# Performance work log

Hardware: AMD Instinct MI355X
Metric: run time of the kernel (lower is better)

## Reference

```python
import jax, jax.numpy as jnp
import numpy as np

N, D, DH, H = 2048, 256, 256, 4
DHEAD = DH // H
NEG = -1e30


def setup_inputs() -> dict:
    key = jax.random.key(0)
    ks = jax.random.split(key, 24)
    s = 0.05
    inp = {
        'axiom_states': jax.random.normal(ks[0], (N, D), jnp.float32),
        'adj0': (jax.random.uniform(ks[1], (N, N)) < 0.015).astype(jnp.float32),
        'adj1': (jax.random.uniform(ks[2], (N, N)) < 0.015).astype(jnp.float32),
        'w0': jax.random.uniform(ks[3], (N, N), jnp.float32),
        'w1': jax.random.uniform(ks[4], (N, N), jnp.float32),
        'Wm0': jax.random.normal(ks[5], (DH, D), jnp.float32) * s,
        'bm0': jax.random.normal(ks[6], (DH,), jnp.float32) * s,
        'Wa0': jax.random.normal(ks[7], (H, 2 * D), jnp.float32) * s,
        'ba0': jax.random.normal(ks[8], (H,), jnp.float32) * s,
        'Wm1': jax.random.normal(ks[9], (DH, D), jnp.float32) * s,
        'bm1': jax.random.normal(ks[10], (DH,), jnp.float32) * s,
        'Wa1': jax.random.normal(ks[11], (H, 2 * D), jnp.float32) * s,
        'ba1': jax.random.normal(ks[12], (H,), jnp.float32) * s,
        'gru_wih': jax.random.normal(ks[13], (3 * D, 2 * DH), jnp.float32) * s,
        'gru_whh': jax.random.normal(ks[14], (3 * D, D), jnp.float32) * s,
        'gru_bih': jax.random.normal(ks[15], (3 * D,), jnp.float32) * s,
        'gru_bhh': jax.random.normal(ks[16], (3 * D,), jnp.float32) * s,
        'ln_g': jnp.ones((D,), jnp.float32),
        'ln_b': jnp.zeros((D,), jnp.float32),
    }
    return inp


def _edge_messages(x, adj, w, Wm, bm, Wa, ba):
    # GAT-style decomposition of Linear([x_i, x_j]) -> a_cur[i] + a_nb[j] + b
    a_cur = x @ Wa[:, :D].T                      # [N,H] (target i, first half of concat)
    a_nb = x @ Wa[:, D:].T                       # [N,H] (neighbor j, second half)
    s = a_nb[:, None, :] + a_cur[None, :, :] + ba  # [j,i,H]
    s = jax.nn.leaky_relu(s, 0.2)
    s = s * w[:, :, None]                        # edge-weight scaled scores (pre-softmax)
    mask = adj != 0                              # edge j -> i iff adj[j,i] != 0
    logits = jnp.where(mask[:, :, None], s, NEG)
    attn = jax.nn.softmax(logits, axis=0) * mask[:, :, None]  # zero for isolated nodes
    msg = (x @ Wm.T + bm).reshape(N, H, DHEAD)   # per-neighbor messages
    agg = jnp.einsum('jih,jhd->ihd', attn, msg)  # softmax-weighted sum over neighbors
    return agg.reshape(N, DH)


def _forward(axiom_states, adj0, adj1, w0, w1, Wm0, bm0, Wa0, ba0,
             Wm1, bm1, Wa1, ba1, gru_wih, gru_whh, gru_bih, gru_bhh, ln_g, ln_b):
    m0 = _edge_messages(axiom_states, adj0, w0, Wm0, bm0, Wa0, ba0)
    m1 = _edge_messages(axiom_states, adj1, w1, Wm1, bm1, Wa1, ba1)
    msg = jnp.concatenate([m0, m1], axis=-1)     # dropout is identity in eval
    # GRUCell (torch semantics)
    gi = msg @ gru_wih.T + gru_bih
    gh = axiom_states @ gru_whh.T + gru_bhh
    r = jax.nn.sigmoid(gi[:, :D] + gh[:, :D])
    z = jax.nn.sigmoid(gi[:, D:2 * D] + gh[:, D:2 * D])
    n = jnp.tanh(gi[:, 2 * D:] + r * gh[:, 2 * D:])
    h = (1.0 - z) * n + z * axiom_states
    # LayerNorm
    mu = jnp.mean(h, axis=-1, keepdims=True)
    var = jnp.var(h, axis=-1, keepdims=True)
    return (h - mu) * jax.lax.rsqrt(var + 1e-5) * ln_g + ln_b


def reference(axiom_states, adj0, adj1, w0, w1, Wm0, bm0, Wa0, ba0,
              Wm1, bm1, Wa1, ba1, gru_wih, gru_whh, gru_bih, gru_bhh, ln_g, ln_b):
    return _forward(axiom_states, adj0, adj1, w0, w1, Wm0, bm0, Wa0, ba0,
                    Wm1, bm1, Wa1, ba1, gru_wih, gru_whh, gru_bih, gru_bhh, ln_g, ln_b)
```

## Files before the change

### kernel.cpp

```cpp
#include <hip/hip_runtime.h>

#define NN 2048
#define DD 256
#define HH 4
#define ECAP 128

typedef unsigned short ushort_t;
typedef __attribute__((ext_vector_type(4))) unsigned short us4;
typedef __attribute__((ext_vector_type(8))) unsigned short us8;
typedef __attribute__((ext_vector_type(8))) short s8;
typedef __attribute__((ext_vector_type(4))) float f4;

__device__ __forceinline__ ushort_t f2b(float f) {
    unsigned int u = __float_as_uint(f);
    return (ushort_t)((u + 0x7fffu + ((u >> 16) & 1u)) >> 16);
}
__device__ __forceinline__ float b2f(ushort_t b) {
    return __uint_as_float(((unsigned int)b) << 16);
}
__device__ __forceinline__ void gl_lds16(const void* g, void* l) {
    __builtin_amdgcn_global_load_lds(
        (const __attribute__((address_space(1))) void*)g,
        (__attribute__((address_space(3))) void*)l, 16, 0, 0);
}

__device__ __forceinline__ void gemm_core_db(
    const ushort_t* __restrict__ A, int lda, const ushort_t* __restrict__ B, int ldb,
    int r0, int c0, int K, ushort_t (*as)[64], ushort_t (*bs)[64], f4 acc[2][2])
{
    const int t = threadIdx.x;
    const int wave = t >> 6, lane = t & 63;
    const int wm = (wave & 1) * 32, wn = (wave >> 1) * 32;
    const int fm = lane & 15, fq = lane >> 4;

    const int m0q0 = wave * 16 + (lane >> 3);
    const int m0q1 = m0q0 + 8;
    const int cs0 = ((lane & 7) ^ (m0q0 & 7)) * 8;
    const int cs1 = ((lane & 7) ^ (m0q1 & 7)) * 8;
    const ushort_t* ga0 = A + (size_t)(r0 + m0q0) * lda + cs0;
    const ushort_t* ga1 = A + (size_t)(r0 + m0q1) * lda + cs1;
    const ushort_t* gb0 = B + (size_t)(c0 + m0q0) * ldb + cs0;
    const ushort_t* gb1 = B + (size_t)(c0 + m0q1) * ldb + cs1;
    const int ra0 = wm + fm, ra1 = wm + 16 + fm;
    const int rb0 = wn + fm, rb1 = wn + 16 + fm;

    gl_lds16(ga0, &as[wave * 16][0]);
    gl_lds16(ga1, &as[wave * 16 + 8][0]);
    gl_lds16(gb0, &bs[wave * 16][0]);
    gl_lds16(gb1, &bs[wave * 16 + 8][0]);
    __syncthreads();

    int buf = 0;
    for (int k0 = 0; k0 < K; k0 += 64) {
        const int nb = buf ^ 64;
        if (k0 + 64 < K) {
            gl_lds16(ga0 + k0 + 64, &as[nb + wave * 16][0]);
            gl_lds16(ga1 + k0 + 64, &as[nb + wave * 16 + 8][0]);
            gl_lds16(gb0 + k0 + 64, &bs[nb + wave * 16][0]);
            gl_lds16(gb1 + k0 + 64, &bs[nb + wave * 16 + 8][0]);
        }
        #pragma unroll
        for (int kk = 0; kk < 2; ++kk) {
            const int cc = kk * 4 + fq;
            const s8 a0 = *(const s8*)&as[buf + ra0][(cc ^ (ra0 & 7)) * 8];
            const s8 a1 = *(const s8*)&as[buf + ra1][(cc ^ (ra1 & 7)) * 8];
            const s8 b0 = *(const s8*)&bs[buf + rb0][(cc ^ (rb0 & 7)) * 8];
            const s8 b1 = *(const s8*)&bs[buf + rb1][(cc ^ (rb1 & 7)) * 8];
            acc[0][0] = __builtin_amdgcn_mfma_f32_16x16x32_bf16(a0, b0, acc[0][0], 0, 0, 0);
            acc[0][1] = __builtin_amdgcn_mfma_f32_16x16x32_bf16(a0, b1, acc[0][1], 0, 0, 0);
            acc[1][0] = __builtin_amdgcn_mfma_f32_16x16x32_bf16(a1, b0, acc[1][0], 0, 0, 0);
            acc[1][1] = __builtin_amdgcn_mfma_f32_16x16x32_bf16(a1, b1, acc[1][1], 0, 0, 0);
        }
        __syncthreads();
        buf = nb;
    }
}

__device__ __forceinline__ us8 cvt8(float4 a, float4 b) {
    us8 o;
    o[0] = f2b(a.x); o[1] = f2b(a.y); o[2] = f2b(a.z); o[3] = f2b(a.w);
    o[4] = f2b(b.x); o[5] = f2b(b.y); o[6] = f2b(b.z); o[7] = f2b(b.w);
    return o;
}

__device__ __forceinline__ void gemm_core_f32(
    const float* __restrict__ A, int lda, const float* __restrict__ B, int ldb,
    int r0, int c0, int K, ushort_t (*as)[64], ushort_t (*bs)[64], f4 acc[2][2])
{
    const int t = threadIdx.x;
    const int wave = t >> 6, lane = t & 63;
    const int wm = (wave & 1) * 32, wn = (wave >> 1) * 32;
    const int fm = lane & 15, fq = lane >> 4;

    const int m1 = wave * 16 + (lane >> 3);
    const int m2 = m1 + 8;
    const int g1 = ((lane & 7) ^ (m1 & 7)) * 8;
    const int g2 = ((lane & 7) ^ (m2 & 7)) * 8;
    const int cl = (lane & 7) * 8;
    const int ra0 = wm + fm, ra1 = wm + 16 + fm;
    const int rb0 = wn + fm, rb1 = wn + 16 + fm;

    const float* pa1 = A + (size_t)(r0 + m1) * lda + g1;
    const float* pa2 = A + (size_t)(r0 + m2) * lda + g2;
    const float* pb1 = B + (size_t)(c0 + m1) * ldb + g1;
    const float* pb2 = B + (size_t)(c0 + m2) * ldb + g2;

    float4 aa0 = *(const float4*)(pa1);
    float4 aa1 = *(const float4*)(pa1 + 4);
    float4 ab0 = *(const float4*)(pa2);
    float4 ab1 = *(const float4*)(pa2 + 4);
    float4 ba0 = *(const float4*)(pb1);
    float4 ba1 = *(const float4*)(pb1 + 4);
    float4 bb0 = *(const float4*)(pb2);
    float4 bb1 = *(const float4*)(pb2 + 4);

    for (int k0 = 0; k0 < K; k0 += 64) {
        __syncthreads();
        *(us8*)&as[m1][cl] = cvt8(aa0, aa1);
        *(us8*)&as[m2][cl] = cvt8(ab0, ab1);
        *(us8*)&bs[m1][cl] = cvt8(ba0, ba1);
        *(us8*)&bs[m2][cl] = cvt8(bb0, bb1);
        __syncthreads();
        if (k0 + 64 < K) {
            aa0 = *(const float4*)(pa1 + k0 + 64);
            aa1 = *(const float4*)(pa1 + k0 + 68);
            ab0 = *(const float4*)(pa2 + k0 + 64);
            ab1 = *(const float4*)(pa2 + k0 + 68);
            ba0 = *(const float4*)(pb1 + k0 + 64);
            ba1 = *(const float4*)(pb1 + k0 + 68);
            bb0 = *(const float4*)(pb2 + k0 + 64);
            bb1 = *(const float4*)(pb2 + k0 + 68);
        }
        #pragma unroll
        for (int kk = 0; kk < 2; ++kk) {
            const int cc = kk * 4 + fq;
            const s8 a0 = *(const s8*)&as[ra0][(cc ^ (ra0 & 7)) * 8];
            const s8 a1 = *(const s8*)&as[ra1][(cc ^ (ra1 & 7)) * 8];
            const s8 b0 = *(const s8*)&bs[rb0][(cc ^ (rb0 & 7)) * 8];
            const s8 b1 = *(const s8*)&bs[rb1][(cc ^ (rb1 & 7)) * 8];
            acc[0][0] = __builtin_amdgcn_mfma_f32_16x16x32_bf16(a0, b0, acc[0][0], 0, 0, 0);
            acc[0][1] = __builtin_amdgcn_mfma_f32_16x16x32_bf16(a0, b1, acc[0][1], 0, 0, 0);
            acc[1][0] = __builtin_amdgcn_mfma_f32_16x16x32_bf16(a1, b0, acc[1][0], 0, 0, 0);
            acc[1][1] = __builtin_amdgcn_mfma_f32_16x16x32_bf16(a1, b1, acc[1][1], 0, 0, 0);
        }
    }
}

#define E_SC  256
#define E_AP  384
#define E_WI  768
#define E_NB  1408

__global__ __launch_bounds__(256) void fused1_kernel(
    const float* __restrict__ x,
    const float* __restrict__ adj0, const float* __restrict__ adj1,
    const float* __restrict__ Wm0, const float* __restrict__ Wm1,
    const float* __restrict__ whh, const float* __restrict__ wih,
    const float* __restrict__ Wa0, const float* __restrict__ Wa1,
    const float* __restrict__ bm0, const float* __restrict__ bm1,
    const float* __restrict__ bhh,
    int* __restrict__ cnt, int* __restrict__ ej,
    ushort_t* __restrict__ wihb,
    float* __restrict__ acur, float* __restrict__ anb,
    ushort_t* __restrict__ msgb, float* __restrict__ gh)
{
    __shared__ char smem[16448];
    const int b = blockIdx.x, t = threadIdx.x;

    if (b < E_SC) {
        const int l = b & 1, chunk = b >> 1;
        const int i0 = chunk * 16;
        const float* adj = l ? adj1 : adj0;
        int* lcnt = (int*)smem;
        if (t < 16) lcnt[t] = 0;
        __syncthreads();
        const int rowLane = t >> 2, q = t & 3;
        for (int r0r = 0; r0r < NN; r0r += 512) {
            float4 a[8];
            #pragma unroll
            for (int it = 0; it < 8; ++it) {
                const int j = r0r + it * 64 + rowLane;
                a[it] = *(const float4*)(adj + (size_t)j * NN + i0 + q * 4);
            }
            #pragma unroll
            for (int it = 0; it < 8; ++it) {
                const int j = r0r + it * 64 + rowLane;
                const float av[4] = {a[it].x, a[it].y, a[it].z, a[it].w};
                #pragma unroll
                for (int u = 0; u < 4; ++u) {
                    if (av[u] != 0.f) {
                        const int li = q * 4 + u;
                        const int slot = atomicAdd(&lcnt[li], 1);
                        if (slot < ECAP)
                            ej[((size_t)l * NN + i0 + li) * ECAP + slot] = j;
                    }
                }
            }
        }
        __syncthreads();
        if (t < 16) cnt[l * NN + i0 + t] = min(lcnt[t], ECAP);
        return;
    }
    if (b < E_AP) {
        float* sh = (float*)smem;
        const int i0 = (b - E_SC) * 16;
        for (int rr = 0; rr < 16; ++rr)
            sh[rr * 257 + t] = x[(size_t)(i0 + rr) * DD + t];
        __syncthreads();
        const int r = t >> 4, idx = t & 15;
        const int l = idx >> 3, isnb = (idx >> 2) & 1, h = idx & 3;
        const float* wrow = (l ? Wa1 : Wa0) + h * (2 * DD) + isnb * DD;
        float acc = 0.f;
        for (int k = 0; k < DD; ++k) acc = fmaf(sh[r * 257 + k], wrow[k], acc);
        float* dst = isnb ? anb : acur;
        dst[((size_t)l * NN + i0 + r) * HH + h] = acc;
        return;
    }
    if (b < E_WI) {
        const int id = (b - E_AP) * 1024 + t * 4;
        const float4 v = *(const float4*)(wih + id);
        us4 o; o.x = f2b(v.x); o.y = f2b(v.y); o.z = f2b(v.z); o.w = f2b(v.w);
        *(us4*)(wihb + id) = o;
        return;
    }
    {
        ushort_t (*as)[64] = (ushort_t(*)[64])smem;
        ushort_t (*bs)[64] = (ushort_t(*)[64])(smem + 8192);
        const int wave = t >> 6, lane = t & 63;
        const int wm = (wave & 1) * 32, wn = (wave >> 1) * 32;
        const int fm = lane & 15, fq = lane >> 4;
        const int idx = b - E_WI;
        const int c0 = (idx % 20) * 64, r0 = (idx / 20) * 64;
        const float* Bsrc = (c0 < 256) ? Wm0 + (size_t)c0 * DD
                          : (c0 < 512) ? Wm1 + (size_t)(c0 - 256) * DD
                                       : whh + (size_t)(c0 - 512) * DD;
        f4 acc[2][2] = {};
        gemm_core_f32(x, DD, Bsrc, DD, r0, 0, DD, as, bs, acc);
        #pragma unroll
        for (int ni = 0; ni < 2; ++ni) {
            const int col = c0 + wn + ni * 16 + fm;
            const float bv = (col < 256) ? bm0[col]
                           : (col < 512) ? bm1[col - 256]
                                         : bhh[col - 512];
            #pragma unroll
            for (int mi = 0; mi < 2; ++mi) {
                #pragma unroll
                for (int r = 0; r < 4; ++r) {
                    const int row = r0 + wm + mi * 16 + fq * 4 + r;
                    const float v = acc[mi][ni][r] + bv;
                    if (col < 512) msgb[(size_t)row * 512 + col] = f2b(v);
                    else           gh[(size_t)row * 768 + col - 512] = v;
                }
            }
        }
    }
}

__global__ __launch_bounds__(256) void attn_kernel(
    const int* __restrict__ cnt, const int* __restrict__ ej,
    const float* __restrict__ w0, const float* __restrict__ w1,
    const float* __restrict__ acur, const float* __restrict__ anb,
    const float* __restrict__ ba0, const float* __restrict__ ba1,
    const ushort_t* __restrict__ msgb, ushort_t* __restrict__ mcatb)
{
    const int i = blockIdx.x, l = blockIdx.y, t = threadIdx.x;
    __shared__ float es[HH][ECAP];
    __shared__ int ejs[ECAP];
    const int ne = min(max(cnt[l * NN + i], 0), ECAP);
    const float* ba = l ? ba1 : ba0;
    const float* w  = l ? w1 : w0;
    const size_t ebase = ((size_t)l * NN + i) * ECAP;

    if (t < ne) {
        const int j = ej[ebase + t];
        const float wv = w[(size_t)j * NN + i];
        ejs[t] = j;
        const float4 av = *(const float4*)(anb + ((size_t)l * NN + j) * HH);
        const float sv[4] = {av.x, av.y, av.z, av.w};
        #pragma unroll
        for (int h = 0; h < HH; ++h) {
            float s = sv[h] + acur[((size_t)l * NN + i) * HH + h] + ba[h];
            s = (s > 0.f) ? s : 0.2f * s;
            es[h][t] = s * wv;
        }
    }
    __syncthreads();
    {
        const int h = t >> 6, lane = t & 63;
        float s0 = (lane < ne) ? es[h][lane] : -1e30f;
        float s1 = (lane + 64 < ne) ? es[h][lane + 64] : -1e30f;
        float m = fmaxf(s0, s1);
        #pragma unroll
        for (int off = 32; off; off >>= 1) m = fmaxf(m, __shfl_xor(m, off));
        const float p0 = expf(s0 - m), p1 = expf(s1 - m);
        float sum = p0 + p1;
        #pragma unroll
        for (int off = 32; off; off >>= 1) sum += __shfl_xor(sum, off);
        const float inv = (ne > 0) ? 1.f / sum : 0.f;
        es[h][lane] = p0 * inv;
        if (lane + 64 < ECAP) es[h][lane + 64] = p1 * inv;
    }
    __syncthreads();
    const int h = t >> 6;
    const int off = l * DD + t;
    float acc = 0.f;
    int e = 0;
    for (; e + 8 <= ne; e += 8) {
        float v[8];
        #pragma unroll
        for (int u = 0; u < 8; ++u)
            v[u] = b2f(msgb[(size_t)ejs[e + u] * 512 + off]);
        #pragma unroll
        for (int u = 0; u < 8; ++u)
            acc = fmaf(es[h][e + u], v[u], acc);
    }
    for (; e < ne; ++e)
        acc = fmaf(es[h][e], b2f(msgb[(size_t)ejs[e] * 512 + off]), acc);
    mcatb[(size_t)i * (2 * DD) + off] = f2b(acc);
}

__global__ __launch_bounds__(256) void gemm2_kernel(
    const ushort_t* __restrict__ mcatb, const ushort_t* __restrict__ wihb,
    const float* __restrict__ bih, float* __restrict__ gi)
{
    __shared__ ushort_t as[128][64];
    __shared__ ushort_t bs[128][64];
    const int t = threadIdx.x;
    const int wave = t >> 6, lane = t & 63;
    const int wm = (wave & 1) * 32, wn = (wave >> 1) * 32;
    const int fm = lane & 15, fq = lane >> 4;
    const int c0 = blockIdx.x * 64, r0 = blockIdx.y * 64;
    f4 acc[2][2] = {};
    gemm_core_db(mcatb, 512, wihb, 512, r0, c0, 512, as, bs, acc);
    #pragma unroll
    for (int ni = 0; ni < 2; ++ni) {
        const int col = c0 + wn + ni * 16 + fm;
        const float bv = bih[col];
        #pragma unroll
        for (int mi = 0; mi < 2; ++mi)
            #pragma unroll
            for (int r = 0; r < 4; ++r)
                gi[(size_t)(r0 + wm + mi * 16 + fq * 4 + r) * 768 + col] =
                    acc[mi][ni][r] + bv;
    }
}

__global__ __launch_bounds__(256) void gates_ln(
    const float* __restrict__ gi, const float* __restrict__ gh, const float* __restrict__ x,
    const float* __restrict__ lng, const float* __restrict__ lnb, float* __restrict__ out)
{
    const int t = threadIdx.x;
    const int lane = t & 63, wv = t >> 6;
    const int row = blockIdx.x * 4 + wv;
    const size_t b768 = (size_t)row * 768;
    const int c = lane * 4;
    const f4 gir = *(const f4*)(gi + b768 + c);
    const f4 giz = *(const f4*)(gi + b768 + 256 + c);
    const f4 gin = *(const f4*)(gi + b768 + 512 + c);
    const f4 ghr = *(const f4*)(gh + b768 + c);
    const f4 ghz = *(const f4*)(gh + b768 + 256 + c);
    const f4 ghn = *(const f4*)(gh + b768 + 512 + c);
    const f4 xv  = *(const f4*)(x + (size_t)row * DD + c);
    f4 hv;
    float s1 = 0.f, s2 = 0.f;
    #pragma unroll
    for (int u = 0; u < 4; ++u) {
        const float rr = 1.f / (1.f + expf(-(gir[u] + ghr[u])));
        const float zz = 1.f / (1.f + expf(-(giz[u] + ghz[u])));
        const float nn = tanhf(gin[u] + rr * ghn[u]);
        const float h = (1.f - zz) * nn + zz * xv[u];
        hv[u] = h;
        s1 += h;
        s2 += h * h;
    }
    #pragma unroll
    for (int off = 32; off; off >>= 1) {
        s1 += __shfl_xor(s1, off);
        s2 += __shfl_xor(s2, off);
    }
    const float mu  = s1 * (1.f / DD);
    const float var = s2 * (1.f / DD) - mu * mu;
    const float inv = rsqrtf(var + 1e-5f);
    const f4 gv = *(const f4*)(lng + c);
    const f4 bv = *(const f4*)(lnb + c);
    f4 res;
    #pragma unroll
    for (int u = 0; u < 4; ++u)
        res[u] = (hv[u] - mu) * inv * gv[u] + bv[u];
    *(f4*)(out + (size_t)row * DD + c) = res;
}

extern "C" void kernel_launch(void* const* d_in, const int* in_sizes, int n_in,
                              void* d_out, int out_size, void* d_ws, size_t ws_size,
                              hipStream_t stream)
{
    const float* x    = (const float*)d_in[0];
    const float* adj0 = (const float*)d_in[1];
    const float* adj1 = (const float*)d_in[2];
    const float* w0   = (const float*)d_in[3];
    const float* w1   = (const float*)d_in[4];
    const float* Wm0  = (const float*)d_in[5];
    const float* bm0  = (const float*)d_in[6];
    const float* Wa0  = (const float*)d_in[7];
    const float* ba0  = (const float*)d_in[8];
    const float* Wm1  = (const float*)d_in[9];
    const float* bm1  = (const float*)d_in[10];
    const float* Wa1  = (const float*)d_in[11];
    const float* ba1  = (const float*)d_in[12];
    const float* wih  = (const float*)d_in[13];
    const float* whh  = (const float*)d_in[14];
    const float* bih  = (const float*)d_in[15];
    const float* bhh  = (const float*)d_in[16];
    const float* lng  = (const float*)d_in[17];
    const float* lnb  = (const float*)d_in[18];
    float* out = (float*)d_out;

    float* ws = (float*)d_ws;
    float* gh   = ws;            ws += (size_t)NN * 768;
    float* gi   = ws;            ws += (size_t)NN * 768;
    float* acur = ws;            ws += 2 * NN * HH;
    float* anb  = ws;            ws += 2 * NN * HH;
    int*   cnt  = (int*)ws;      ws += 2 * NN;
    int*   ej   = (int*)ws;      ws += 2 * NN * ECAP;
    ushort_t* wihb  = (ushort_t*)ws;  ws += (size_t)768 * 512 / 2;
    ushort_t* msgb  = (ushort_t*)ws;  ws += (size_t)NN * 512 / 2;
    ushort_t* mcatb = (ushort_t*)ws;  ws += (size_t)NN * 512 / 2;

    fused1_kernel<<<E_NB, 256, 0, stream>>>(
        x, adj0, adj1, Wm0, Wm1, whh, wih, Wa0, Wa1, bm0, bm1, bhh,
        cnt, ej, wihb, acur, anb, msgb, gh);
    attn_kernel<<<dim3(NN, 2), 256, 0, stream>>>(
        cnt, ej, w0, w1, acur, anb, ba0, ba1, msgb, mcatb);
    gemm2_kernel<<<dim3(12, 32), 256, 0, stream>>>(mcatb, wihb, bih, gi);
    gates_ln<<<NN / 4, 256, 0, stream>>>(gi, gh, x, lng, lnb, out);
}
```

Baseline: 167.6 us.

## Merge four kernels into one persistent kernel with grid-wide barriers

```diff
diff --git a/kernel.cpp b/kernel.cpp
--- a/kernel.cpp
+++ b/kernel.cpp
@@ -4,6 +4,7 @@
 #define DD 256
 #define HH 4
 #define ECAP 128
+#define NBLK 512
 
 typedef unsigned short ushort_t;
 typedef __attribute__((ext_vector_type(4))) unsigned short us4;
@@ -22,6 +23,18 @@
     __builtin_amdgcn_global_load_lds(
         (const __attribute__((address_space(1))) void*)g,
         (__attribute__((address_space(3))) void*)l, 16, 0, 0);
+}
+
+__device__ __forceinline__ void gsync(int* bar) {
+    __threadfence();
+    __syncthreads();
+    if (threadIdx.x == 0) {
+        __hip_atomic_fetch_add(bar, 1, __ATOMIC_ACQ_REL, __HIP_MEMORY_SCOPE_AGENT);
+        while (__hip_atomic_load(bar, __ATOMIC_ACQUIRE, __HIP_MEMORY_SCOPE_AGENT) < NBLK)
+            __builtin_amdgcn_s_sleep(1);
+    }
+    __syncthreads();
+    __threadfence();
 }
 
 __device__ __forceinline__ void gemm_core_db(
@@ -151,243 +164,273 @@
 #define E_WI  768
 #define E_NB  1408
 
-__global__ __launch_bounds__(256) void fused1_kernel(
+__global__ __launch_bounds__(256, 2) void mega_kernel(
     const float* __restrict__ x,
     const float* __restrict__ adj0, const float* __restrict__ adj1,
+    const float* __restrict__ w0, const float* __restrict__ w1,
     const float* __restrict__ Wm0, const float* __restrict__ Wm1,
     const float* __restrict__ whh, const float* __restrict__ wih,
     const float* __restrict__ Wa0, const float* __restrict__ Wa1,
     const float* __restrict__ bm0, const float* __restrict__ bm1,
     const float* __restrict__ bhh,
+    const float* __restrict__ ba0, const float* __restrict__ ba1,
+    const float* __restrict__ bih,
+    const float* __restrict__ lng, const float* __restrict__ lnb,
     int* __restrict__ cnt, int* __restrict__ ej,
     ushort_t* __restrict__ wihb,
     float* __restrict__ acur, float* __restrict__ anb,
-    ushort_t* __restrict__ msgb, float* __restrict__ gh)
+    ushort_t* __restrict__ msgb, ushort_t* __restrict__ mcatb,
+    float* __restrict__ gh, float* __restrict__ gi,
+    float* __restrict__ out, int* __restrict__ bar)
 {
-    __shared__ char smem[16448];
-    const int b = blockIdx.x, t = threadIdx.x;
-
-    if (b < E_SC) {
-        const int l = b & 1, chunk = b >> 1;
-        const int i0 = chunk * 16;
-        const float* adj = l ? adj1 : adj0;
-        int* lcnt = (int*)smem;
-        if (t < 16) lcnt[t] = 0;
+    __shared__ __align__(16) char smem[32768];
+    const int rb = blockIdx.x, t = threadIdx.x;
+
+    for (int vb = rb; vb < E_NB; vb += NBLK) {
+        if (vb < E_SC) {
+            const int l = vb & 1, chunk = vb >> 1;
+            const int i0 = chunk * 16;
+            const float* adj = l ? adj1 : adj0;
+            int* lcnt = (int*)smem;
+            if (t < 16) lcnt[t] = 0;
+            __syncthreads();
+            const int rowLane = t >> 2, q = t & 3;
+            for (int r0r = 0; r0r < NN; r0r += 512) {
+                float4 a[8];
+                #pragma unroll
+                for (int it = 0; it < 8; ++it) {
+                    const int j = r0r + it * 64 + rowLane;
+                    a[it] = *(const float4*)(adj + (size_t)j * NN + i0 + q * 4);
+                }
+                #pragma unroll
+                for (int it = 0; it < 8; ++it) {
+                    const int j = r0r + it * 64 + rowLane;
+                    const float av[4] = {a[it].x, a[it].y, a[it].z, a[it].w};
+                    #pragma unroll
+                    for (int u = 0; u < 4; ++u) {
+                        if (av[u] != 0.f) {
+                            const int li = q * 4 + u;
+                            const int slot = atomicAdd(&lcnt[li], 1);
+                            if (slot < ECAP)
+                                ej[((size_t)l * NN + i0 + li) * ECAP + slot] = j;
+                        }
+                    }
+                }
+            }
+            __syncthreads();
+            if (t < 16) cnt[l * NN + i0 + t] = min(lcnt[t], ECAP);
+        } else if (vb < E_AP) {
+            float* sh = (float*)smem;
+            const int i0 = (vb - E_SC) * 16;
+            for (int rr = 0; rr < 16; ++rr)
+                sh[rr * 257 + t] = x[(size_t)(i0 + rr) * DD + t];
+            __syncthreads();
+            const int r = t >> 4, idx = t & 15;
+            const int l = idx >> 3, isnb = (idx >> 2) & 1, h = idx & 3;
+            const float* wrow = (l ? Wa1 : Wa0) + h * (2 * DD) + isnb * DD;
+            float acc = 0.f;
+            for (int k = 0; k < DD; ++k) acc = fmaf(sh[r * 257 + k], wrow[k], acc);
+            float* dst = isnb ? anb : acur;
+            dst[((size_t)l * NN + i0 + r) * HH + h] = acc;
+        } else if (vb < E_WI) {
+            const int id = (vb - E_AP) * 1024 + t * 4;
+            const float4 v = *(const float4*)(wih + id);
+            us4 o; o.x = f2b(v.x); o.y = f2b(v.y); o.z = f2b(v.z); o.w = f2b(v.w);
+            *(us4*)(wihb + id) = o;
+        } else {
+            ushort_t (*as)[64] = (ushort_t(*)[64])smem;
+            ushort_t (*bs)[64] = (ushort_t(*)[64])(smem + 8192);
+            const int wave = t >> 6, lane = t & 63;
+            const int wm = (wave & 1) * 32, wn = (wave >> 1) * 32;
+            const int fm = lane & 15, fq = lane >> 4;
+            const int idx = vb - E_WI;
+            const int c0 = (idx % 20) * 64, r0 = (idx / 20) * 64;
+            const float* Bsrc = (c0 < 256) ? Wm0 + (size_t)c0 * DD
+                              : (c0 < 512) ? Wm1 + (size_t)(c0 - 256) * DD
+                                           : whh + (size_t)(c0 - 512) * DD;
+            f4 acc[2][2] = {};
+            gemm_core_f32(x, DD, Bsrc, DD, r0, 0, DD, as, bs, acc);
+            #pragma unroll
+            for (int ni = 0; ni < 2; ++ni) {
+                const int col = c0 + wn + ni * 16 + fm;
+                const float bv = (col < 256) ? bm0[col]
+                               : (col < 512) ? bm1[col - 256]
+                                             : bhh[col - 512];
+                #pragma unroll
+                for (int mi = 0; mi < 2; ++mi) {
+                    #pragma unroll
+                    for (int r = 0; r < 4; ++r) {
+                        const int row = r0 + wm + mi * 16 + fq * 4 + r;
+                        const float v = acc[mi][ni][r] + bv;
+                        if (col < 512) msgb[(size_t)row * 512 + col] = f2b(v);
+                        else           gh[(size_t)row * 768 + col - 512] = v;
+                    }
+                }
+            }
+        }
         __syncthreads();
-        const int rowLane = t >> 2, q = t & 3;
-        for (int r0r = 0; r0r < NN; r0r += 512) {
-            float4 a[8];
+    }
+    gsync(bar + 0);
+
+    {
+        const int wave = t >> 6, lane = t & 63;
+        float (*esw)[ECAP] = (float(*)[ECAP])smem + wave * HH;
+        int* ejs = (int*)(smem + 8192) + wave * ECAP;
+        for (int it = 0; it < 2; ++it) {
+            const int pair = it * 2048 + rb * 4 + wave;
+            const int i = pair & (NN - 1), l = pair >> 11;
+            const int ne = min(max(cnt[l * NN + i], 0), ECAP);
+            const float* ba = l ? ba1 : ba0;
+            const float* w  = l ? w1 : w0;
+            const size_t ebase = ((size_t)l * NN + i) * ECAP;
+            float acv[4];
             #pragma unroll
-            for (int it = 0; it < 8; ++it) {
-                const int j = r0r + it * 64 + rowLane;
-                a[it] = *(const float4*)(adj + (size_t)j * NN + i0 + q * 4);
+            for (int h = 0; h < HH; ++h)
+                acv[h] = acur[((size_t)l * NN + i) * HH + h];
+
+            float s0[HH], s1[HH];
+            int j0 = 0, j1 = 0;
+            if (lane < ne) {
+                j0 = ej[ebase + lane];
+                const float wv = w[(size_t)j0 * NN + i];
+                const float4 av = *(const float4*)(anb + ((size_t)l * NN + j0) * HH);
+                const float sv[4] = {av.x, av.y, av.z, av.w};
+                #pragma unroll
+                for (int h = 0; h < HH; ++h) {
+                    float s = sv[h] + acv[h] + ba[h];
+                    s = (s > 0.f) ? s : 0.2f * s;
+                    s0[h] = s * wv;
+                }
+            } else {
+                #pragma unroll
+                for (int h = 0; h < HH; ++h) s0[h] = -1e30f;
+            }
+            if (lane + 64 < ne) {
+                j1 = ej[ebase + lane + 64];
+                const float wv = w[(size_t)j1 * NN + i];
+                const float4 av = *(const float4*)(anb + ((size_t)l * NN + j1) * HH);
+                const float sv[4] = {av.x, av.y, av.z, av.w};
+                #pragma unroll
+                for (int h = 0; h < HH; ++h) {
+                    float s = sv[h] + acv[h] + ba[h];
+                    s = (s > 0.f) ? s : 0.2f * s;
+                    s1[h] = s * wv;
+                }
+            } else {
+                #pragma unroll
+                for (int h = 0; h < HH; ++h) s1[h] = -1e30f;
             }
             #pragma unroll
-            for (int it = 0; it < 8; ++it) {
-                const int j = r0r + it * 64 + rowLane;
-                const float av[4] = {a[it].x, a[it].y, a[it].z, a[it].w};
-                #pragma unroll
-                for (int u = 0; u < 4; ++u) {
-                    if (av[u] != 0.f) {
-                        const int li = q * 4 + u;
-                        const int slot = atomicAdd(&lcnt[li], 1);
-                        if (slot < ECAP)
-                            ej[((size_t)l * NN + i0 + li) * ECAP + slot] = j;
-                    }
-                }
-            }
-        }
-        __syncthreads();
-        if (t < 16) cnt[l * NN + i0 + t] = min(lcnt[t], ECAP);
-        return;
-    }
-    if (b < E_AP) {
-        float* sh = (float*)smem;
-        const int i0 = (b - E_SC) * 16;
-        for (int rr = 0; rr < 16; ++rr)
-            sh[rr * 257 + t] = x[(size_t)(i0 + rr) * DD + t];
-        __syncthreads();
-        const int r = t >> 4, idx = t & 15;
-        const int l = idx >> 3, isnb = (idx >> 2) & 1, h = idx & 3;
-        const float* wrow = (l ? Wa1 : Wa0) + h * (2 * DD) + isnb * DD;
-        float acc = 0.f;
-        for (int k = 0; k < DD; ++k) acc = fmaf(sh[r * 257 + k], wrow[k], acc);
-        float* dst = isnb ? anb : acur;
-        dst[((size_t)l * NN + i0 + r) * HH + h] = acc;
-        return;
-    }
-    if (b < E_WI) {
-        const int id = (b - E_AP) * 1024 + t * 4;
-        const float4 v = *(const float4*)(wih + id);
-        us4 o; o.x = f2b(v.x); o.y = f2b(v.y); o.z = f2b(v.z); o.w = f2b(v.w);
-        *(us4*)(wihb + id) = o;
-        return;
-    }
-    {
+            for (int h = 0; h < HH; ++h) {
+                float m = fmaxf(s0[h], s1[h]);
+                #pragma unroll
+                for (int off = 32; off; off >>= 1) m = fmaxf(m, __shfl_xor(m, off));
+                const float p0 = expf(s0[h] - m), p1 = expf(s1[h] - m);
+                float sum = p0 + p1;
+                #pragma unroll
+                for (int off = 32; off; off >>= 1) sum += __shfl_xor(sum, off);
+                const float inv = (ne > 0) ? 1.f / sum : 0.f;
+                esw[h][lane] = p0 * inv;
+                esw[h][lane + 64] = p1 * inv;
+            }
+            ejs[lane] = j0;
+            ejs[lane + 64] = j1;
+            const int h = lane >> 4;
+            const size_t obase = (size_t)(l * DD) + lane * 4;
+            float a0 = 0.f, a1 = 0.f, a2 = 0.f, a3 = 0.f;
+            int e = 0;
+            for (; e + 8 <= ne; e += 8) {
+                int jv[8]; float pv[8]; us4 mv[8];
+                #pragma unroll
+                for (int u = 0; u < 8; ++u) { jv[u] = ejs[e + u]; pv[u] = esw[h][e + u]; }
+                #pragma unroll
+                for (int u = 0; u < 8; ++u)
+                    mv[u] = *(const us4*)&msgb[(size_t)jv[u] * 512 + obase];
+                #pragma unroll
+                for (int u = 0; u < 8; ++u) {
+                    a0 = fmaf(pv[u], b2f(mv[u].x), a0);
+                    a1 = fmaf(pv[u], b2f(mv[u].y), a1);
+                    a2 = fmaf(pv[u], b2f(mv[u].z), a2);
+                    a3 = fmaf(pv[u], b2f(mv[u].w), a3);
+                }
+            }
+            for (; e < ne; ++e) {
+                const us4 mv = *(const us4*)&msgb[(size_t)ejs[e] * 512 + obase];
+                const float pe = esw[h][e];
+                a0 = fmaf(pe, b2f(mv.x), a0);
+                a1 = fmaf(pe, b2f(mv.y), a1);
+                a2 = fmaf(pe, b2f(mv.z), a2);
+                a3 = fmaf(pe, b2f(mv.w), a3);
+            }
+            us4 o; o.x = f2b(a0); o.y = f2b(a1); o.z = f2b(a2); o.w = f2b(a3);
+            *(us4*)&mcatb[(size_t)i * (2 * DD) + obase] = o;
+        }
+    }
+    gsync(bar + 1);
+
+    if (rb < 384) {
         ushort_t (*as)[64] = (ushort_t(*)[64])smem;
-        ushort_t (*bs)[64] = (ushort_t(*)[64])(smem + 8192);
+        ushort_t (*bs)[64] = (ushort_t(*)[64])(smem + 16384);
         const int wave = t >> 6, lane = t & 63;
         const int wm = (wave & 1) * 32, wn = (wave >> 1) * 32;
         const int fm = lane & 15, fq = lane >> 4;
-        const int idx = b - E_WI;
-        const int c0 = (idx % 20) * 64, r0 = (idx / 20) * 64;
-        const float* Bsrc = (c0 < 256) ? Wm0 + (size_t)c0 * DD
-                          : (c0 < 512) ? Wm1 + (size_t)(c0 - 256) * DD
-                                       : whh + (size_t)(c0 - 512) * DD;
+        const int c0 = (rb % 12) * 64, r0 = (rb / 12) * 64;
         f4 acc[2][2] = {};
-        gemm_core_f32(x, DD, Bsrc, DD, r0, 0, DD, as, bs, acc);
+        gemm_core_db(mcatb, 512, wihb, 512, r0, c0, 512, as, bs, acc);
         #pragma unroll
         for (int ni = 0; ni < 2; ++ni) {
             const int col = c0 + wn + ni * 16 + fm;
-            const float bv = (col < 256) ? bm0[col]
-                           : (col < 512) ? bm1[col - 256]
-                                         : bhh[col - 512];
+            const float bv = bih[col];
             #pragma unroll
-            for (int mi = 0; mi < 2; ++mi) {
-                #pragma unroll
-                for (int r = 0; r < 4; ++r) {
-                    const int row = r0 + wm + mi * 16 + fq * 4 + r;
-                    const float v = acc[mi][ni][r] + bv;
-                    if (col < 512) msgb[(size_t)row * 512 + col] = f2b(v);
-                    else           gh[(size_t)row * 768 + col - 512] = v;
-                }
-            }
-        }
-    }
-}
-
-__global__ __launch_bounds__(256) void attn_kernel(
-    const int* __restrict__ cnt, const int* __restrict__ ej,
-    const float* __restrict__ w0, const float* __restrict__ w1,
-    const float* __restrict__ acur, const float* __restrict__ anb,
-    const float* __restrict__ ba0, const float* __restrict__ ba1,
-    const ushort_t* __restrict__ msgb, ushort_t* __restrict__ mcatb)
-{
-    const int i = blockIdx.x, l = blockIdx.y, t = threadIdx.x;
-    __shared__ float es[HH][ECAP];
-    __shared__ int ejs[ECAP];
-    const int ne = min(max(cnt[l * NN + i], 0), ECAP);
-    const float* ba = l ? ba1 : ba0;
-    const float* w  = l ? w1 : w0;
-    const size_t ebase = ((size_t)l * NN + i) * ECAP;
-
-    if (t < ne) {
-        const int j = ej[ebase + t];
-        const float wv = w[(size_t)j * NN + i];
-        ejs[t] = j;
-        const float4 av = *(const float4*)(anb + ((size_t)l * NN + j) * HH);
-        const float sv[4] = {av.x, av.y, av.z, av.w};
-        #pragma unroll
-        for (int h = 0; h < HH; ++h) {
-            float s = sv[h] + acur[((size_t)l * NN + i) * HH + h] + ba[h];
-            s = (s > 0.f) ? s : 0.2f * s;
-            es[h][t] = s * wv;
-        }
-    }
-    __syncthreads();
+            for (int mi = 0; mi < 2; ++mi)
+                #pragma unroll
+                for (int r = 0; r < 4; ++r)
+                    gi[(size_t)(r0 + wm + mi * 16 + fq * 4 + r) * 768 + col] =
+                        acc[mi][ni][r] + bv;
+        }
+    }
+    gsync(bar + 2);
+
     {
-        const int h = t >> 6, lane = t & 63;
-        float s0 = (lane < ne) ? es[h][lane] : -1e30f;
-        float s1 = (lane + 64 < ne) ? es[h][lane + 64] : -1e30f;
-        float m = fmaxf(s0, s1);
-        #pragma unroll
-        for (int off = 32; off; off >>= 1) m = fmaxf(m, __shfl_xor(m, off));
-        const float p0 = expf(s0 - m), p1 = expf(s1 - m);
-        float sum = p0 + p1;
-        #pragma unroll
-        for (int off = 32; off; off >>= 1) sum += __shfl_xor(sum, off);
-        const float inv = (ne > 0) ? 1.f / sum : 0.f;
-        es[h][lane] = p0 * inv;
-        if (lane + 64 < ECAP) es[h][lane + 64] = p1 * inv;
-    }
-    __syncthreads();
-    const int h = t >> 6;
-    const int off = l * DD + t;
-    float acc = 0.f;
-    int e = 0;
-    for (; e + 8 <= ne; e += 8) {
-        float v[8];
-        #pragma unroll
-        for (int u = 0; u < 8; ++u)
-            v[u] = b2f(msgb[(size_t)ejs[e + u] * 512 + off]);
-        #pragma unroll
-        for (int u = 0; u < 8; ++u)
-            acc = fmaf(es[h][e + u], v[u], acc);
-    }
-    for (; e < ne; ++e)
-        acc = fmaf(es[h][e], b2f(msgb[(size_t)ejs[e] * 512 + off]), acc);
-    mcatb[(size_t)i * (2 * DD) + off] = f2b(acc);
-}
-
-__global__ __launch_bounds__(256) void gemm2_kernel(
-    const ushort_t* __restrict__ mcatb, const ushort_t* __restrict__ wihb,
-    const float* __restrict__ bih, float* __restrict__ gi)
-{
-    __shared__ ushort_t as[128][64];
-    __shared__ ushort_t bs[128][64];
-    const int t = threadIdx.x;
-    const int wave = t >> 6, lane = t & 63;
-    const int wm = (wave & 1) * 32, wn = (wave >> 1) * 32;
-    const int fm = lane & 15, fq = lane >> 4;
-    const int c0 = blockIdx.x * 64, r0 = blockIdx.y * 64;
-    f4 acc[2][2] = {};
-    gemm_core_db(mcatb, 512, wihb, 512, r0, c0, 512, as, bs, acc);
-    #pragma unroll
-    for (int ni = 0; ni < 2; ++ni) {
-        const int col = c0 + wn + ni * 16 + fm;
-        const float bv = bih[col];
-        #pragma unroll
-        for (int mi = 0; mi < 2; ++mi)
-            #pragma unroll
-            for (int r = 0; r < 4; ++r)
-                gi[(size_t)(r0 + wm + mi * 16 + fq * 4 + r) * 768 + col] =
-                    acc[mi][ni][r] + bv;
-    }
-}
-
-__global__ __launch_bounds__(256) void gates_ln(
-    const float* __restrict__ gi, const float* __restrict__ gh, const float* __restrict__ x,
-    const float* __restrict__ lng, const float* __restrict__ lnb, float* __restrict__ out)
-{
-    const int t = threadIdx.x;
-    const int lane = t & 63, wv = t >> 6;
-    const int row = blockIdx.x * 4 + wv;
-    const size_t b768 = (size_t)row * 768;
-    const int c = lane * 4;
-    const f4 gir = *(const f4*)(gi + b768 + c);
-    const f4 giz = *(const f4*)(gi + b768 + 256 + c);
-    const f4 gin = *(const f4*)(gi + b768 + 512 + c);
-    const f4 ghr = *(const f4*)(gh + b768 + c);
-    const f4 ghz = *(const f4*)(gh + b768 + 256 + c);
-    const f4 ghn = *(const f4*)(gh + b768 + 512 + c);
-    const f4 xv  = *(const f4*)(x + (size_t)row * DD + c);
-    f4 hv;
-    float s1 = 0.f, s2 = 0.f;
-    #pragma unroll
-    for (int u = 0; u < 4; ++u) {
-        const float rr = 1.f / (1.f + expf(-(gir[u] + ghr[u])));
-        const float zz = 1.f / (1.f + expf(-(giz[u] + ghz[u])));
-        const float nn = tanhf(gin[u] + rr * ghn[u]);
-        const float h = (1.f - zz) * nn + zz * xv[u];
-        hv[u] = h;
-        s1 += h;
-        s2 += h * h;
-    }
-    #pragma unroll
-    for (int off = 32; off; off >>= 1) {
-        s1 += __shfl_xor(s1, off);
-        s2 += __shfl_xor(s2, off);
-    }
-    const float mu  = s1 * (1.f / DD);
-    const float var = s2 * (1.f / DD) - mu * mu;
-    const float inv = rsqrtf(var + 1e-5f);
-    const f4 gv = *(const f4*)(lng + c);
-    const f4 bv = *(const f4*)(lnb + c);
-    f4 res;
-    #pragma unroll
-    for (int u = 0; u < 4; ++u)
-        res[u] = (hv[u] - mu) * inv * gv[u] + bv[u];
-    *(f4*)(out + (size_t)row * DD + c) = res;
+        const int lane = t & 63, wv = t >> 6;
+        const int row = rb * 4 + wv;
+        const size_t b768 = (size_t)row * 768;
+        const int c = lane * 4;
+        const f4 gir = *(const f4*)(gi + b768 + c);
+        const f4 giz = *(const f4*)(gi + b768 + 256 + c);
+        const f4 gin = *(const f4*)(gi + b768 + 512 + c);
+        const f4 ghr = *(const f4*)(gh + b768 + c);
+        const f4 ghz = *(const f4*)(gh + b768 + 256 + c);
+        const f4 ghn = *(const f4*)(gh + b768 + 512 + c);
+        const f4 xv  = *(const f4*)(x + (size_t)row * DD + c);
+        f4 hv;
+        float s1 = 0.f, s2 = 0.f;
+        #pragma unroll
+        for (int u = 0; u < 4; ++u) {
+            const float rr = 1.f / (1.f + expf(-(gir[u] + ghr[u])));
+            const float zz = 1.f / (1.f + expf(-(giz[u] + ghz[u])));
+            const float nn = tanhf(gin[u] + rr * ghn[u]);
+            const float h = (1.f - zz) * nn + zz * xv[u];
+            hv[u] = h;
+            s1 += h;
+            s2 += h * h;
+        }
+        #pragma unroll
+        for (int off = 32; off; off >>= 1) {
+            s1 += __shfl_xor(s1, off);
+            s2 += __shfl_xor(s2, off);
+        }
+        const float mu  = s1 * (1.f / DD);
+        const float var = s2 * (1.f / DD) - mu * mu;
+        const float inv = rsqrtf(var + 1e-5f);
+        const f4 gv = *(const f4*)(lng + c);
+        const f4 bv = *(const f4*)(lnb + c);
+        f4 res;
+        #pragma unroll
+        for (int u = 0; u < 4; ++u)
+            res[u] = (hv[u] - mu) * inv * gv[u] + bv[u];
+        *(f4*)(out + (size_t)row * DD + c) = res;
+    }
 }
 
 extern "C" void kernel_launch(void* const* d_in, const int* in_sizes, int n_in,
@@ -425,12 +468,11 @@
     ushort_t* wihb  = (ushort_t*)ws;  ws += (size_t)768 * 512 / 2;
     ushort_t* msgb  = (ushort_t*)ws;  ws += (size_t)NN * 512 / 2;
     ushort_t* mcatb = (ushort_t*)ws;  ws += (size_t)NN * 512 / 2;
-
-    fused1_kernel<<<E_NB, 256, 0, stream>>>(
-        x, adj0, adj1, Wm0, Wm1, whh, wih, Wa0, Wa1, bm0, bm1, bhh,
-        cnt, ej, wihb, acur, anb, msgb, gh);
-    attn_kernel<<<dim3(NN, 2), 256, 0, stream>>>(
-        cnt, ej, w0, w1, acur, anb, ba0, ba1, msgb, mcatb);
-    gemm2_kernel<<<dim3(12, 32), 256, 0, stream>>>(mcatb, wihb, bih, gi);
-    gates_ln<<<NN / 4, 256, 0, stream>>>(gi, gh, x, lng, lnb, out);
-}
+    int* bar = (int*)ws;         ws += 16;
+
+    hipMemsetAsync(bar, 0, 3 * sizeof(int), stream);
+    mega_kernel<<<NBLK, 256, 0, stream>>>(
+        x, adj0, adj1, w0, w1, Wm0, Wm1, whh, wih, Wa0, Wa1,
+        bm0, bm1, bhh, ba0, ba1, bih, lng, lnb,
+        cnt, ej, wihb, acur, anb, msgb, mcatb, gh, gi, out, bar);
+}
```

Measured after the change: 597.0 us. +256.3%, slower.

## Fuse GRU gates and LayerNorm into GEMM via last-block-per-row-tile counter

Applied to the files above, without the earlier changes.

```diff
diff --git a/kernel.cpp b/kernel.cpp
--- a/kernel.cpp
+++ b/kernel.cpp
@@ -319,12 +319,16 @@
     mcatb[(size_t)i * (2 * DD) + off] = f2b(acc);
 }
 
-__global__ __launch_bounds__(256) void gemm2_kernel(
+__global__ __launch_bounds__(256) void gemm2_gates(
     const ushort_t* __restrict__ mcatb, const ushort_t* __restrict__ wihb,
-    const float* __restrict__ bih, float* __restrict__ gi)
+    const float* __restrict__ bih, float* __restrict__ gi,
+    const float* __restrict__ gh, const float* __restrict__ x,
+    const float* __restrict__ lng, const float* __restrict__ lnb,
+    float* __restrict__ out, int* __restrict__ tilecnt)
 {
     __shared__ ushort_t as[128][64];
     __shared__ ushort_t bs[128][64];
+    __shared__ int last_flag;
     const int t = threadIdx.x;
     const int wave = t >> 6, lane = t & 63;
     const int wm = (wave & 1) * 32, wn = (wave >> 1) * 32;
@@ -343,51 +347,56 @@
                 gi[(size_t)(r0 + wm + mi * 16 + fq * 4 + r) * 768 + col] =
                     acc[mi][ni][r] + bv;
     }
-}
-
-__global__ __launch_bounds__(256) void gates_ln(
-    const float* __restrict__ gi, const float* __restrict__ gh, const float* __restrict__ x,
-    const float* __restrict__ lng, const float* __restrict__ lnb, float* __restrict__ out)
-{
-    const int t = threadIdx.x;
-    const int lane = t & 63, wv = t >> 6;
-    const int row = blockIdx.x * 4 + wv;
-    const size_t b768 = (size_t)row * 768;
+    __syncthreads();
+    if (t == 0) {
+        __threadfence();
+        const int old = __hip_atomic_fetch_add(&tilecnt[blockIdx.y], 1,
+                           __ATOMIC_ACQ_REL, __HIP_MEMORY_SCOPE_AGENT);
+        if (old == 11) __threadfence();
+        last_flag = (old == 11);
+    }
+    __syncthreads();
+    if (!last_flag) return;
+
     const int c = lane * 4;
-    const f4 gir = *(const f4*)(gi + b768 + c);
-    const f4 giz = *(const f4*)(gi + b768 + 256 + c);
-    const f4 gin = *(const f4*)(gi + b768 + 512 + c);
-    const f4 ghr = *(const f4*)(gh + b768 + c);
-    const f4 ghz = *(const f4*)(gh + b768 + 256 + c);
-    const f4 ghn = *(const f4*)(gh + b768 + 512 + c);
-    const f4 xv  = *(const f4*)(x + (size_t)row * DD + c);
-    f4 hv;
-    float s1 = 0.f, s2 = 0.f;
-    #pragma unroll
-    for (int u = 0; u < 4; ++u) {
-        const float rr = 1.f / (1.f + expf(-(gir[u] + ghr[u])));
-        const float zz = 1.f / (1.f + expf(-(giz[u] + ghz[u])));
-        const float nn = tanhf(gin[u] + rr * ghn[u]);
-        const float h = (1.f - zz) * nn + zz * xv[u];
-        hv[u] = h;
-        s1 += h;
-        s2 += h * h;
-    }
-    #pragma unroll
-    for (int off = 32; off; off >>= 1) {
-        s1 += __shfl_xor(s1, off);
-        s2 += __shfl_xor(s2, off);
-    }
-    const float mu  = s1 * (1.f / DD);
-    const float var = s2 * (1.f / DD) - mu * mu;
-    const float inv = rsqrtf(var + 1e-5f);
     const f4 gv = *(const f4*)(lng + c);
-    const f4 bv = *(const f4*)(lnb + c);
-    f4 res;
-    #pragma unroll
-    for (int u = 0; u < 4; ++u)
-        res[u] = (hv[u] - mu) * inv * gv[u] + bv[u];
-    *(f4*)(out + (size_t)row * DD + c) = res;
+    const f4 bvv = *(const f4*)(lnb + c);
+    for (int it = 0; it < 16; ++it) {
+        const int row = r0 + wave * 16 + it;
+        const size_t b768 = (size_t)row * 768;
+        const f4 gir = *(const f4*)(gi + b768 + c);
+        const f4 giz = *(const f4*)(gi + b768 + 256 + c);
+        const f4 gin = *(const f4*)(gi + b768 + 512 + c);
+        const f4 ghr = *(const f4*)(gh + b768 + c);
+        const f4 ghz = *(const f4*)(gh + b768 + 256 + c);
+        const f4 ghn = *(const f4*)(gh + b768 + 512 + c);
+        const f4 xv  = *(const f4*)(x + (size_t)row * DD + c);
+        f4 hv;
+        float s1 = 0.f, s2 = 0.f;
+        #pragma unroll
+        for (int u = 0; u < 4; ++u) {
+            const float rr = 1.f / (1.f + expf(-(gir[u] + ghr[u])));
+            const float zz = 1.f / (1.f + expf(-(giz[u] + ghz[u])));
+            const float nn = tanhf(gin[u] + rr * ghn[u]);
+            const float h = (1.f - zz) * nn + zz * xv[u];
+            hv[u] = h;
+            s1 += h;
+            s2 += h * h;
+        }
+        #pragma unroll
+        for (int off = 32; off; off >>= 1) {
+            s1 += __shfl_xor(s1, off);
+            s2 += __shfl_xor(s2, off);
+        }
+        const float mu  = s1 * (1.f / DD);
+        const float var = s2 * (1.f / DD) - mu * mu;
+        const float inv = rsqrtf(var + 1e-5f);
+        f4 res;
+        #pragma unroll
+        for (int u = 0; u < 4; ++u)
+            res[u] = (hv[u] - mu) * inv * gv[u] + bvv[u];
+        *(f4*)(out + (size_t)row * DD + c) = res;
+    }
 }
 
 extern "C" void kernel_launch(void* const* d_in, const int* in_sizes, int n_in,
@@ -425,12 +434,14 @@
     ushort_t* wihb  = (ushort_t*)ws;  ws += (size_t)768 * 512 / 2;
     ushort_t* msgb  = (ushort_t*)ws;  ws += (size_t)NN * 512 / 2;
     ushort_t* mcatb = (ushort_t*)ws;  ws += (size_t)NN * 512 / 2;
-
+    int* tilecnt = (int*)ws;     ws += 32;
+
+    hipMemsetAsync(tilecnt, 0, 32 * sizeof(int), stream);
     fused1_kernel<<<E_NB, 256, 0, stream>>>(
         x, adj0, adj1, Wm0, Wm1, whh, wih, Wa0, Wa1, bm0, bm1, bhh,
         cnt, ej, wihb, acur, anb, msgb, gh);
     attn_kernel<<<dim3(NN, 2), 256, 0, stream>>>(
         cnt, ej, w0, w1, acur, anb, ba0, ba1, msgb, mcatb);
-    gemm2_kernel<<<dim3(12, 32), 256, 0, stream>>>(mcatb, wihb, bih, gi);
-    gates_ln<<<NN / 4, 256, 0, stream>>>(gi, gh, x, lng, lnb, out);
-}
+    gemm2_gates<<<dim3(12, 32), 256, 0, stream>>>(
+        mcatb, wihb, bih, gi, gh, x, lng, lnb, out, tilecnt);
+}
```

Measured after the change: 216.0 us. 28.9% more time.

## Move wih bf16 conversion into attention kernel and enlarge gemm2 tiles

Applied to the files above, without the earlier changes.

```diff
diff --git a/kernel.cpp b/kernel.cpp
--- a/kernel.cpp
+++ b/kernel.cpp
@@ -22,58 +22,6 @@
     __builtin_amdgcn_global_load_lds(
         (const __attribute__((address_space(1))) void*)g,
         (__attribute__((address_space(3))) void*)l, 16, 0, 0);
-}
-
-__device__ __forceinline__ void gemm_core_db(
-    const ushort_t* __restrict__ A, int lda, const ushort_t* __restrict__ B, int ldb,
-    int r0, int c0, int K, ushort_t (*as)[64], ushort_t (*bs)[64], f4 acc[2][2])
-{
-    const int t = threadIdx.x;
-    const int wave = t >> 6, lane = t & 63;
-    const int wm = (wave & 1) * 32, wn = (wave >> 1) * 32;
-    const int fm = lane & 15, fq = lane >> 4;
-
-    const int m0q0 = wave * 16 + (lane >> 3);
-    const int m0q1 = m0q0 + 8;
-    const int cs0 = ((lane & 7) ^ (m0q0 & 7)) * 8;
-    const int cs1 = ((lane & 7) ^ (m0q1 & 7)) * 8;
-    const ushort_t* ga0 = A + (size_t)(r0 + m0q0) * lda + cs0;
-    const ushort_t* ga1 = A + (size_t)(r0 + m0q1) * lda + cs1;
-    const ushort_t* gb0 = B + (size_t)(c0 + m0q0) * ldb + cs0;
-    const ushort_t* gb1 = B + (size_t)(c0 + m0q1) * ldb + cs1;
-    const int ra0 = wm + fm, ra1 = wm + 16 + fm;
-    const int rb0 = wn + fm, rb1 = wn + 16 + fm;
-
-    gl_lds16(ga0, &as[wave * 16][0]);
-    gl_lds16(ga1, &as[wave * 16 + 8][0]);
-    gl_lds16(gb0, &bs[wave * 16][0]);
-    gl_lds16(gb1, &bs[wave * 16 + 8][0]);
-    __syncthreads();
-
-    int buf = 0;
-    for (int k0 = 0; k0 < K; k0 += 64) {
-        const int nb = buf ^ 64;
-        if (k0 + 64 < K) {
-            gl_lds16(ga0 + k0 + 64, &as[nb + wave * 16][0]);
-            gl_lds16(ga1 + k0 + 64, &as[nb + wave * 16 + 8][0]);
-            gl_lds16(gb0 + k0 + 64, &bs[nb + wave * 16][0]);
-            gl_lds16(gb1 + k0 + 64, &bs[nb + wave * 16 + 8][0]);
-        }
-        #pragma unroll
-        for (int kk = 0; kk < 2; ++kk) {
-            const int cc = kk * 4 + fq;
-            const s8 a0 = *(const s8*)&as[buf + ra0][(cc ^ (ra0 & 7)) * 8];
-            const s8 a1 = *(const s8*)&as[buf + ra1][(cc ^ (ra1 & 7)) * 8];
-            const s8 b0 = *(const s8*)&bs[buf + rb0][(cc ^ (rb0 & 7)) * 8];
-            const s8 b1 = *(const s8*)&bs[buf + rb1][(cc ^ (rb1 & 7)) * 8];
-            acc[0][0] = __builtin_amdgcn_mfma_f32_16x16x32_bf16(a0, b0, acc[0][0], 0, 0, 0);
-            acc[0][1] = __builtin_amdgcn_mfma_f32_16x16x32_bf16(a0, b1, acc[0][1], 0, 0, 0);
-            acc[1][0] = __builtin_amdgcn_mfma_f32_16x16x32_bf16(a1, b0, acc[1][0], 0, 0, 0);
-            acc[1][1] = __builtin_amdgcn_mfma_f32_16x16x32_bf16(a1, b1, acc[1][1], 0, 0, 0);
-        }
-        __syncthreads();
-        buf = nb;
-    }
 }
 
 __device__ __forceinline__ us8 cvt8(float4 a, float4 b) {
@@ -148,19 +96,17 @@
 
 #define E_SC  256
 #define E_AP  384
-#define E_WI  768
-#define E_NB  1408
+#define E_NB  1024
 
 __global__ __launch_bounds__(256) void fused1_kernel(
     const float* __restrict__ x,
     const float* __restrict__ adj0, const float* __restrict__ adj1,
     const float* __restrict__ Wm0, const float* __restrict__ Wm1,
-    const float* __restrict__ whh, const float* __restrict__ wih,
+    const float* __restrict__ whh,
     const float* __restrict__ Wa0, const float* __restrict__ Wa1,
     const float* __restrict__ bm0, const float* __restrict__ bm1,
     const float* __restrict__ bhh,
     int* __restrict__ cnt, int* __restrict__ ej,
-    ushort_t* __restrict__ wihb,
     float* __restrict__ acur, float* __restrict__ anb,
     ushort_t* __restrict__ msgb, float* __restrict__ gh)
 {
@@ -216,20 +162,13 @@
         dst[((size_t)l * NN + i0 + r) * HH + h] = acc;
         return;
     }
-    if (b < E_WI) {
-        const int id = (b - E_AP) * 1024 + t * 4;
-        const float4 v = *(const float4*)(wih + id);
-        us4 o; o.x = f2b(v.x); o.y = f2b(v.y); o.z = f2b(v.z); o.w = f2b(v.w);
-        *(us4*)(wihb + id) = o;
-        return;
-    }
     {
         ushort_t (*as)[64] = (ushort_t(*)[64])smem;
         ushort_t (*bs)[64] = (ushort_t(*)[64])(smem + 8192);
         const int wave = t >> 6, lane = t & 63;
         const int wm = (wave & 1) * 32, wn = (wave >> 1) * 32;
         const int fm = lane & 15, fq = lane >> 4;
-        const int idx = b - E_WI;
+        const int idx = b - E_AP;
         const int c0 = (idx % 20) * 64, r0 = (idx / 20) * 64;
         const float* Bsrc = (c0 < 256) ? Wm0 + (size_t)c0 * DD
                           : (c0 < 512) ? Wm1 + (size_t)(c0 - 256) * DD
@@ -261,11 +200,23 @@
     const float* __restrict__ w0, const float* __restrict__ w1,
     const float* __restrict__ acur, const float* __restrict__ anb,
     const float* __restrict__ ba0, const float* __restrict__ ba1,
-    const ushort_t* __restrict__ msgb, ushort_t* __restrict__ mcatb)
+    const ushort_t* __restrict__ msgb, ushort_t* __restrict__ mcatb,
+    const float* __restrict__ wih, ushort_t* __restrict__ wihb)
 {
     const int i = blockIdx.x, l = blockIdx.y, t = threadIdx.x;
     __shared__ float es[HH][ECAP];
     __shared__ int ejs[ECAP];
+
+    {
+        const int fb = i + (l << 11);
+        if (t < 24) {
+            const int id = fb * 96 + t * 4;
+            const float4 v = *(const float4*)(wih + id);
+            us4 o; o.x = f2b(v.x); o.y = f2b(v.y); o.z = f2b(v.z); o.w = f2b(v.w);
+            *(us4*)(wihb + id) = o;
+        }
+    }
+
     const int ne = min(max(cnt[l * NN + i], 0), ECAP);
     const float* ba = l ? ba1 : ba0;
     const float* w  = l ? w1 : w0;
@@ -323,18 +274,68 @@
     const ushort_t* __restrict__ mcatb, const ushort_t* __restrict__ wihb,
     const float* __restrict__ bih, float* __restrict__ gi)
 {
-    __shared__ ushort_t as[128][64];
+    __shared__ ushort_t as[256][64];
     __shared__ ushort_t bs[128][64];
     const int t = threadIdx.x;
     const int wave = t >> 6, lane = t & 63;
-    const int wm = (wave & 1) * 32, wn = (wave >> 1) * 32;
+    const int wm = wave * 32;
     const int fm = lane & 15, fq = lane >> 4;
-    const int c0 = blockIdx.x * 64, r0 = blockIdx.y * 64;
-    f4 acc[2][2] = {};
-    gemm_core_db(mcatb, 512, wihb, 512, r0, c0, 512, as, bs, acc);
-    #pragma unroll
-    for (int ni = 0; ni < 2; ++ni) {
-        const int col = c0 + wn + ni * 16 + fm;
+    const int c0 = blockIdx.x * 64, r0 = blockIdx.y * 128;
+
+    const int lr = lane >> 3;
+    const int swz = ((lane & 7) ^ lr) * 8;
+    const ushort_t* gaA[4];
+    const ushort_t* gaB[2];
+    #pragma unroll
+    for (int g = 0; g < 4; ++g)
+        gaA[g] = mcatb + (size_t)(r0 + wm + g * 8 + lr) * 512 + swz;
+    #pragma unroll
+    for (int g = 0; g < 2; ++g)
+        gaB[g] = wihb + (size_t)(c0 + wave * 16 + g * 8 + lr) * 512 + swz;
+
+    f4 acc[2][4] = {};
+
+    #pragma unroll
+    for (int g = 0; g < 4; ++g) gl_lds16(gaA[g], &as[wm + g * 8][0]);
+    #pragma unroll
+    for (int g = 0; g < 2; ++g) gl_lds16(gaB[g], &bs[wave * 16 + g * 8][0]);
+    __syncthreads();
+
+    int abuf = 0, bbuf = 0;
+    for (int k0 = 0; k0 < 512; k0 += 64) {
+        const int na = abuf ^ 128, nb = bbuf ^ 64;
+        if (k0 + 64 < 512) {
+            #pragma unroll
+            for (int g = 0; g < 4; ++g)
+                gl_lds16(gaA[g] + k0 + 64, &as[na + wm + g * 8][0]);
+            #pragma unroll
+            for (int g = 0; g < 2; ++g)
+                gl_lds16(gaB[g] + k0 + 64, &bs[nb + wave * 16 + g * 8][0]);
+        }
+        #pragma unroll
+        for (int kk = 0; kk < 2; ++kk) {
+            const int cc = kk * 4 + fq;
+            const int ce = (cc ^ (fm & 7)) * 8;
+            s8 af[2], bf[4];
+            #pragma unroll
+            for (int mi = 0; mi < 2; ++mi)
+                af[mi] = *(const s8*)&as[abuf + wm + mi * 16 + fm][ce];
+            #pragma unroll
+            for (int ni = 0; ni < 4; ++ni)
+                bf[ni] = *(const s8*)&bs[bbuf + ni * 16 + fm][ce];
+            #pragma unroll
+            for (int mi = 0; mi < 2; ++mi)
+                #pragma unroll
+                for (int ni = 0; ni < 4; ++ni)
+                    acc[mi][ni] = __builtin_amdgcn_mfma_f32_16x16x32_bf16(
+                        af[mi], bf[ni], acc[mi][ni], 0, 0, 0);
+        }
+        __syncthreads();
+        abuf = na; bbuf = nb;
+    }
+    #pragma unroll
+    for (int ni = 0; ni < 4; ++ni) {
+        const int col = c0 + ni * 16 + fm;
         const float bv = bih[col];
         #pragma unroll
         for (int mi = 0; mi < 2; ++mi)
@@ -427,10 +428,10 @@
     ushort_t* mcatb = (ushort_t*)ws;  ws += (size_t)NN * 512 / 2;
 
     fused1_kernel<<<E_NB, 256, 0, stream>>>(
-        x, adj0, adj1, Wm0, Wm1, whh, wih, Wa0, Wa1, bm0, bm1, bhh,
-        cnt, ej, wihb, acur, anb, msgb, gh);
+        x, adj0, adj1, Wm0, Wm1, whh, Wa0, Wa1, bm0, bm1, bhh,
+        cnt, ej, acur, anb, msgb, gh);
     attn_kernel<<<dim3(NN, 2), 256, 0, stream>>>(
-        cnt, ej, w0, w1, acur, anb, ba0, ba1, msgb, mcatb);
-    gemm2_kernel<<<dim3(12, 32), 256, 0, stream>>>(mcatb, wihb, bih, gi);
+        cnt, ej, w0, w1, acur, anb, ba0, ba1, msgb, mcatb, wih, wihb);
+    gemm2_kernel<<<dim3(12, 16), 256, 0, stream>>>(mcatb, wihb, bih, gi);
     gates_ln<<<NN / 4, 256, 0, stream>>>(gi, gh, x, lng, lnb, out);
 }
```

New measurement: 167.6 us. No clear change (+0.0%).
